# Performance work log

Measured on AMD Instinct MI355X. Metric: run time of the kernel, lower is better.

## Reference

```python
import jax, jax.numpy as jnp
import numpy as np

WS = 7        # window size
MAXD = 3      # correlation max displacement -> (2*3+1)^2 = 49 channels
T = 8         # hardcoded temporal length in forward
NUM_HEADS = 8


def setup_inputs() -> dict:
    key = jax.random.key(0)
    ks = jax.random.split(key, 5)
    B, H, W, C = 2, 56, 56, 128
    N = T * H * W
    x = jax.random.normal(ks[0], (B, N, C), jnp.float32)
    qkv_w = jax.random.normal(ks[1], (3 * C, C), jnp.float32) * 0.02
    proj_w = jax.random.normal(ks[2], (C, C), jnp.float32) * 0.02
    proj_b = jnp.zeros((C,), jnp.float32)
    pos_embed1 = jax.random.normal(ks[3], (1, WS * WS, 49), jnp.float32) * 0.02
    pos_embed2 = jax.random.normal(ks[4], (1, WS * WS, C // NUM_HEADS), jnp.float32) * 0.02
    return dict(x=x, qkv_w=qkv_w, proj_w=proj_w, proj_b=proj_b,
                pos_embed1=pos_embed1, pos_embed2=pos_embed2)


def _l2norm(x, axis):
    return x / jnp.maximum(jnp.sqrt(jnp.sum(x * x, axis=axis, keepdims=True)), 1e-12)


def _correlation(a, b):
    # a, b: (B, C, H, W) -> (B, H, W, 49); zero-padded shifted dot products over C
    Bc, Cc, H, W = a.shape
    bp = jnp.pad(b, ((0, 0), (0, 0), (MAXD, MAXD), (MAXD, MAXD)))
    outs = [jnp.sum(a * bp[:, :, du:du + H, dv:dv + W], axis=1)
            for du in range(2 * MAXD + 1) for dv in range(2 * MAXD + 1)]
    return jnp.stack(outs, axis=-1)


def _windows(x):
    # x: (B, H, W, D) -> (B*nh*nw, WS*WS, D); H split as (WS, nh) per torch reshape
    Bc, H, W, D = x.shape
    nh, nw = H // WS, W // WS
    x = x.reshape(Bc, WS, nh, WS, nw, D).transpose(0, 2, 4, 1, 3, 5)
    return x.reshape(Bc * nh * nw, WS * WS, D)


def _unwindows(x, Bc, H, W):
    nh, nw = H // WS, W // WS
    D = x.shape[-1]
    x = x.reshape(Bc, nh, nw, WS, WS, D).transpose(0, 3, 1, 4, 2, 5)
    return x.reshape(Bc, H, W, D)


def reference(x, qkv_w, proj_w, proj_b, pos_embed1, pos_embed2):
    B, N, C = x.shape
    H = int(np.sqrt(N // T)); W = H
    hd = C // NUM_HEADS
    BT = B * NUM_HEADS * T

    qkv = (x @ qkv_w.T).reshape(B, N, 3, NUM_HEADS, hd).transpose(2, 0, 3, 1, 4)
    q, k, v = qkv[0], qkv[1], qkv[2]            # (B, heads, N, hd)

    q = q.reshape(B * NUM_HEADS, T, H, W, hd).transpose(0, 1, 4, 2, 3)  # (B*h, T, hd, H, W)
    k = k.reshape(B * NUM_HEADS, T, H, W, hd).transpose(0, 1, 4, 2, 3)
    v = v.reshape(BT, H * W, hd)

    k_post = jnp.concatenate([k[:, 1:], k[:, -1:]], axis=1)  # shift by one frame
    qp = _l2norm(q.reshape(BT, hd, H, W), axis=1)
    kp = _l2norm(k_post.reshape(BT, hd, H, W), axis=1)

    corr = _correlation(qp, kp)                 # (BT, H, W, 49)
    corr = _windows(corr) + pos_embed1          # (BT*nh*nw, 49, 49)
    motion_attn = jax.nn.softmax(jnp.einsum('bnd,bmd->bnm', corr, corr), axis=-1)

    motion_v = _windows(v.reshape(BT, H, W, hd))
    motion_x = _unwindows(motion_attn @ motion_v, BT, H, W)

    qw = _windows(qp.transpose(0, 2, 3, 1)) + pos_embed2
    app_attn = jax.nn.softmax(jnp.einsum('bnd,bmd->bnm', qw, qw), axis=-1)
    app_x = _unwindows(app_attn @ motion_v, BT, H, W)

    out = 0.5 * app_x + 0.5 * motion_x          # (BT, H, W, hd)
    out = out.reshape(B, NUM_HEADS, T, H, W, hd).transpose(0, 2, 3, 4, 1, 5).reshape(B, N, C)
    return out @ proj_w.T + proj_b
```

## Files before the change

### kernel.cpp

```cpp
#include <hip/hip_runtime.h>
#include <math.h>

constexpr int H_   = 56;
constexpr int HW_  = 56 * 56;
constexpr int NPIX = 8 * HW_;
constexpr int SLAB = 128 * HW_ * 16;
constexpr int CWST = 52;

typedef __attribute__((ext_vector_type(8))) short bf16x8;
typedef __attribute__((ext_vector_type(4))) float f32x4;
typedef __attribute__((ext_vector_type(4))) unsigned int u32x4;

__device__ __forceinline__ unsigned short f2bf(float x) {
  unsigned int u = __float_as_uint(x);
  unsigned int r = (u + 0x7fffu + ((u >> 16) & 1u)) >> 16;
  return (unsigned short)r;
}
__device__ __forceinline__ float bf2f(unsigned short h) {
  return __uint_as_float(((unsigned int)h) << 16);
}

template <int MODE>
__global__ __launch_bounds__(256, 3) void gemm128(
    const float* X, const float* __restrict__ Wt, const float* __restrict__ bias,
    float* __restrict__ Yq, float* __restrict__ Yk, float* __restrict__ Yv,
    float* Yout)
{
  __shared__ float xT[32][132];
  __shared__ float wT[32][132];
  const int tid = threadIdx.x;
  const int tx = tid & 15, ty = tid >> 4;
  const int mbase = blockIdx.x * 128;
  const int nt = (MODE == 0) ? (int)blockIdx.y : 0;
  const float* Wp = Wt + (size_t)nt * (128 * 128);

  float acc[8][8];
#pragma unroll
  for (int i = 0; i < 8; ++i)
#pragma unroll
    for (int j = 0; j < 8; ++j) acc[i][j] = 0.f;

  const int srow = tid >> 3;
  const int scol = (tid & 7) * 4;

  for (int kt = 0; kt < 4; ++kt) {
    if (kt) __syncthreads();
#pragma unroll
    for (int p = 0; p < 4; ++p) {
      int r = p * 32 + srow;
      float4 vx = *(const float4*)&X [(size_t)(mbase + r) * 128 + kt * 32 + scol];
      float4 vw = *(const float4*)&Wp[(size_t)r * 128 + kt * 32 + scol];
      xT[scol + 0][r] = vx.x; xT[scol + 1][r] = vx.y; xT[scol + 2][r] = vx.z; xT[scol + 3][r] = vx.w;
      wT[scol + 0][r] = vw.x; wT[scol + 1][r] = vw.y; wT[scol + 2][r] = vw.z; wT[scol + 3][r] = vw.w;
    }
    __syncthreads();
#pragma unroll 4
    for (int c = 0; c < 32; ++c) {
      float4 a0 = *(const float4*)&xT[c][tx * 4];
      float4 a1 = *(const float4*)&xT[c][64 + tx * 4];
      float4 b0 = *(const float4*)&wT[c][ty * 4];
      float4 b1 = *(const float4*)&wT[c][64 + ty * 4];
      float a[8] = {a0.x, a0.y, a0.z, a0.w, a1.x, a1.y, a1.z, a1.w};
      float b[8] = {b0.x, b0.y, b0.z, b0.w, b1.x, b1.y, b1.z, b1.w};
#pragma unroll
      for (int i = 0; i < 8; ++i)
#pragma unroll
        for (int j = 0; j < 8; ++j) acc[i][j] += a[i] * b[j];
    }
  }

  if (MODE == 0) {
    const int hq = ty >> 2;
    const int cq = (ty & 3) * 4;
    float* Ybase = (nt == 0) ? Yq : ((nt == 1) ? Yk : Yv);
#pragma unroll
    for (int i = 0; i < 8; ++i) {
      int gpix = mbase + ((i < 4) ? (tx * 4 + i) : (64 + tx * 4 + (i - 4)));
      int b = gpix / NPIX;
      int rem = gpix - b * NPIX;
      int t = rem / HW_;
      int s = rem - t * HW_;
      float s0 = acc[i][0]*acc[i][0] + acc[i][1]*acc[i][1] + acc[i][2]*acc[i][2] + acc[i][3]*acc[i][3];
      float s1 = acc[i][4]*acc[i][4] + acc[i][5]*acc[i][5] + acc[i][6]*acc[i][6] + acc[i][7]*acc[i][7];
      s0 += __shfl_xor(s0, 16); s0 += __shfl_xor(s0, 32);
      s1 += __shfl_xor(s1, 16); s1 += __shfl_xor(s1, 32);
      float r0 = 1.f, r1 = 1.f;
      if (nt < 2) {
        r0 = 1.f / fmaxf(sqrtf(s0), 1e-12f);
        r1 = 1.f / fmaxf(sqrtf(s1), 1e-12f);
      }
      int bt0 = (b * 8 + hq) * 8 + t;
      int bt1 = (b * 8 + hq + 4) * 8 + t;
      float* d0 = Ybase + ((size_t)bt0 * HW_ + s) * 16 + cq;
      float* d1 = Ybase + ((size_t)bt1 * HW_ + s) * 16 + cq;
      *(float4*)d0 = make_float4(acc[i][0]*r0, acc[i][1]*r0, acc[i][2]*r0, acc[i][3]*r0);
      *(float4*)d1 = make_float4(acc[i][4]*r1, acc[i][5]*r1, acc[i][6]*r1, acc[i][7]*r1);
    }
  } else {
    float4 bb0 = *(const float4*)&bias[ty * 4];
    float4 bb1 = *(const float4*)&bias[64 + ty * 4];
#pragma unroll
    for (int i = 0; i < 8; ++i) {
      int gpix = mbase + ((i < 4) ? (tx * 4 + i) : (64 + tx * 4 + (i - 4)));
      float* dst = Yout + (size_t)gpix * 128;
      *(float4*)&dst[ty * 4]      = make_float4(acc[i][0]+bb0.x, acc[i][1]+bb0.y, acc[i][2]+bb0.z, acc[i][3]+bb0.w);
      *(float4*)&dst[64 + ty * 4] = make_float4(acc[i][4]+bb1.x, acc[i][5]+bb1.y, acc[i][6]+bb1.z, acc[i][7]+bb1.w);
    }
  }
}

__global__ __launch_bounds__(256) void corr_dense(
    const float* __restrict__ qn, const float* __restrict__ kn,
    const float* __restrict__ pos1,
    unsigned int* __restrict__ cwpk, float* __restrict__ diib)
{
  __shared__ float kS[10][56][16];
  const int bid = blockIdx.x;
  const int xcd = bid & 7;
  const int j = bid >> 3;
  const int g = j / 14;
  const int strip = j - g * 14;
  const int bt = xcd * 16 + g;
  const int h0 = strip * 4;
  const int t = bt & 7;
  const int btk = bt - t + ((t < 7) ? (t + 1) : 7);
  const float* qb = qn + (size_t)bt  * (HW_ * 16);
  const float* kb = kn + (size_t)btk * (HW_ * 16);
  const int tid = threadIdx.x;

  for (int idx = tid; idx < 2240; idx += 256) {
    int r = idx / 224;
    int c = idx - r * 224;
    int hh = h0 - 3 + r;
    f32x4 v = (f32x4)0.f;
    if ((unsigned)hh < 56u)
      v = *(const f32x4*)(kb + (size_t)(hh * 56) * 16 + c * 4);
    *(f32x4*)(&kS[r][0][0] + c * 4) = v;
  }
  __syncthreads();

  if (tid < 224) {
    const int py = tid / 56;
    const int h = h0 + py;
    const int w = tid - py * 56;
    const f32x4* qp = (const f32x4*)(qb + (size_t)(h * 56 + w) * 16);
    f32x4 q0 = qp[0], q1 = qp[1], q2 = qp[2], q3 = qp[3];
    const int ridx = (h >> 3) * 7 + (w >> 3);
    const float* p1r = pos1 + ridx * 49;
    unsigned int* outr = cwpk + (size_t)(bt * HW_ + h * 56 + w) * CWST;
    float dii = 0.f;
#pragma unroll
    for (int d4 = 0; d4 < 12; ++d4) {
      unsigned int pk[4];
#pragma unroll
      for (int e = 0; e < 4; ++e) {
        const int d = d4 * 4 + e;
        const int du = d / 7, dv = d % 7;
        const int ww = w + dv - 3;
        float val = 0.f;
        if (((unsigned)(h + du - 3) < 56u) && ((unsigned)ww < 56u)) {
          const f32x4* kp = (const f32x4*)&kS[py + du][ww][0];
          f32x4 a = q0 * kp[0] + q1 * kp[1] + q2 * kp[2] + q3 * kp[3];
          val = (a.x + a.y) + (a.z + a.w);
        }
        val += p1r[d];
        dii += val * val;
        unsigned short hb = f2bf(val);
        unsigned short lb = f2bf(val - bf2f(hb));
        pk[e] = (unsigned)hb | ((unsigned)lb << 16);
      }
      *(u32x4*)(outr + d4 * 4) = *(const u32x4*)pk;
    }
    {
      const int ww = w + 3;
      float val = 0.f;
      if (((unsigned)(h + 3) < 56u) && ((unsigned)ww < 56u)) {
        const f32x4* kp = (const f32x4*)&kS[py + 6][ww][0];
        f32x4 a = q0 * kp[0] + q1 * kp[1] + q2 * kp[2] + q3 * kp[3];
        val = (a.x + a.y) + (a.z + a.w);
      }
      val += p1r[48];
      dii += val * val;
      unsigned short hb = f2bf(val);
      unsigned short lb = f2bf(val - bf2f(hb));
      outr[48] = (unsigned)hb | ((unsigned)lb << 16);
    }
    diib[bt * HW_ + h * 56 + w] = dii;
  }
}

__global__ __launch_bounds__(64, 2) void attn_mfma(
    const float* __restrict__ qn, const float* __restrict__ vv,
    const unsigned int* __restrict__ cwpk, const float* __restrict__ diib,
    const float* __restrict__ pos2, float* __restrict__ mid)
{
  __shared__ __align__(16) unsigned char smem[7808];
  unsigned short* Pb   = (unsigned short*)smem;
  float*          mi_s = (float*)(smem + 7104);
  float*          scm  = (float*)(smem + 7300);
  float*          sca  = (float*)(smem + 7500);

  const int lane = threadIdx.x;
  const int lg = lane >> 4;
  const int lr = lane & 15;
  const int bid = blockIdx.x;
  const int xcd = bid & 7;
  const int j = bid >> 3;
  const int bt = xcd * 16 + (j >> 6);
  const int win = j & 63;
  const int wy = win >> 3;
  const int wx = win & 7;
  const float* qb = qn + (size_t)bt * (HW_ * 16);
  const float* vb = vv + (size_t)bt * (HW_ * 16);
  const unsigned int* cwb = cwpk + (size_t)bt * HW_ * CWST;
  const float* dib = diib + (size_t)bt * HW_;

  const bool rowok = (lane < 49);
  const int il = rowok ? lane : 48;

  float xv[2][8];
#pragma unroll
  for (int ks = 0; ks < 2; ++ks) {
#pragma unroll
    for (int e = 0; e < 8; ++e) {
      int k = ks * 32 + lg * 8 + e;
      int kc2 = (k < 49) ? k : 0;
      int ka = (kc2 * 37) >> 8;
      int kb2 = kc2 - ka * 7;
      float x = vb[(size_t)((ka * 8 + wy) * 56 + (kb2 * 8 + wx)) * 16 + lr];
      xv[ks][e] = (k < 49) ? x : 0.f;
    }
  }

  {
    const int ia = (il * 37) >> 8;
    const int ib = il - ia * 7;
    float dii = dib[(ia * 8 + wy) * 56 + (ib * 8 + wx)];
    float md = dii;
#pragma unroll
    for (int o = 32; o >= 1; o >>= 1) md = fmaxf(md, __shfl_xor(md, o));
    if (rowok) mi_s[il] = sqrtf(dii * md);
  }

  bf16x8 ah[4][2], al[4][2];
#pragma unroll
  for (int half = 0; half < 2; ++half) {
    u32x4 raw[2][2][2];
#pragma unroll
    for (int u = 0; u < 2; ++u) {
      const int tt2 = half * 2 + u;
      const int row = tt2 * 16 + lr;
      const int rowc = (row < 49) ? row : 0;
      const int a2 = (rowc * 37) >> 8;
      const int b3 = rowc - a2 * 7;
      const unsigned int* src = cwb + (size_t)((a2 * 8 + wy) * 56 + (b3 * 8 + wx)) * CWST;
#pragma unroll
      for (int ks = 0; ks < 2; ++ks) {
        const int cb = ks * 32 + lg * 8;
        raw[u][ks][0] = *(const u32x4*)(src + cb);
        raw[u][ks][1] = *(const u32x4*)(src + cb + 4);
      }
    }
#pragma unroll
    for (int u = 0; u < 2; ++u) {
      const int tt2 = half * 2 + u;
      const int row = tt2 * 16 + lr;
      const bool rv = (row < 49);
#pragma unroll
      for (int ks = 0; ks < 2; ++ks) {
        const int cb = ks * 32 + lg * 8;
        unsigned int u0[8];
        *(u32x4*)&u0[0] = raw[u][ks][0];
        *(u32x4*)&u0[4] = raw[u][ks][1];
#pragma unroll
        for (int e = 0; e < 8; ++e)
          if (!rv || (cb + e) >= 49) u0[e] = 0u;
        union { u32x4 uu; bf16x8 s; } Hh, Ll;
#pragma unroll
        for (int p = 0; p < 4; ++p) {
          Hh.uu[p] = (u0[2*p] & 0xffffu) | (u0[2*p+1] << 16);
          Ll.uu[p] = (u0[2*p] >> 16) | (u0[2*p+1] & 0xffff0000u);
        }
        ah[tt2][ks] = Hh.s;
        al[tt2][ks] = Ll.s;
      }
    }
  }

#pragma unroll
  for (int rt = 0; rt < 4; ++rt) {
    f32x4 C[4];
#pragma unroll
    for (int ct = 0; ct < 4; ++ct) C[ct] = (f32x4)0.f;
#pragma unroll
    for (int ks = 0; ks < 2; ++ks) {
#pragma unroll
      for (int ct = 0; ct < 4; ++ct) {
        C[ct] = __builtin_amdgcn_mfma_f32_16x16x32_bf16(ah[rt][ks], ah[ct][ks], C[ct], 0, 0, 0);
        C[ct] = __builtin_amdgcn_mfma_f32_16x16x32_bf16(ah[rt][ks], al[ct][ks], C[ct], 0, 0, 0);
        C[ct] = __builtin_amdgcn_mfma_f32_16x16x32_bf16(al[rt][ks], ah[ct][ks], C[ct], 0, 0, 0);
      }
    }
#pragma unroll
    for (int reg = 0; reg < 4; ++reg) {
      int row = rt * 16 + lg * 4 + reg;
      float m = mi_s[(row < 49) ? row : 0];
#pragma unroll
      for (int ct = 0; ct < 4; ++ct) {
        float p = __expf(C[ct][reg] - m);
        if (row < 49) Pb[row * 72 + ct * 16 + lr] = f2bf(p);
      }
    }
  }
  asm volatile("" ::: "memory");

  if (rowok) {
    const u32x4* pr = (const u32x4*)(Pb + il * 72);
    unsigned int uu[28];
#pragma unroll
    for (int w = 0; w < 7; ++w) *(u32x4*)&uu[4*w] = pr[w];
    float s = 0.f;
#pragma unroll
    for (int w = 0; w < 24; ++w)
      s += bf2f((unsigned short)(uu[w] & 0xffffu)) + bf2f((unsigned short)(uu[w] >> 16));
    s += bf2f((unsigned short)(uu[24] & 0xffffu));
    scm[il] = 0.5f / s;
  }

  bf16x8 vfh[2], vfl[2];
#pragma unroll
  for (int ks = 0; ks < 2; ++ks) {
    union { u32x4 u; bf16x8 s; } Hh, Ll;
#pragma unroll
    for (int p = 0; p < 4; ++p) {
      unsigned short h0 = f2bf(xv[ks][2*p]);
      unsigned short h1 = f2bf(xv[ks][2*p+1]);
      unsigned short l0 = f2bf(xv[ks][2*p]   - bf2f(h0));
      unsigned short l1 = f2bf(xv[ks][2*p+1] - bf2f(h1));
      Hh.u[p] = (unsigned int)h0 | ((unsigned int)h1 << 16);
      Ll.u[p] = (unsigned int)l0 | ((unsigned int)l1 << 16);
    }
    vfh[ks] = Hh.s;
    vfl[ks] = Ll.s;
  }

  f32x4 om[4];
#pragma unroll
  for (int rt = 0; rt < 4; ++rt) om[rt] = (f32x4)0.f;
#pragma unroll
  for (int ks = 0; ks < 2; ++ks) {
#pragma unroll
    for (int rt = 0; rt < 4; ++rt) {
      int row = rt * 16 + lr;
      int rowc = (row < 49) ? row : 0;
      bf16x8 pa = *(const bf16x8*)(Pb + rowc * 72 + ks * 32 + lg * 8);
      om[rt] = __builtin_amdgcn_mfma_f32_16x16x32_bf16(pa, vfh[ks], om[rt], 0, 0, 0);
      om[rt] = __builtin_amdgcn_mfma_f32_16x16x32_bf16(pa, vfl[ks], om[rt], 0, 0, 0);
    }
  }
  asm volatile("s_waitcnt lgkmcnt(0)" ::: "memory");

  bf16x8 qf[4];
#pragma unroll
  for (int half = 0; half < 2; ++half) {
    f32x4 qa_[2], qb_[2], pa_[2], pb_[2];
#pragma unroll
    for (int u = 0; u < 2; ++u) {
      const int tt2 = half * 2 + u;
      int row = tt2 * 16 + lr;
      int rowc = (row < 49) ? row : 0;
      int a2 = (rowc * 37) >> 8;
      int b3 = rowc - a2 * 7;
      const int co = (lg & 1) * 8;
      const float* qsrc = qb + (size_t)((a2 * 8 + wy) * 56 + (b3 * 8 + wx)) * 16 + co;
      qa_[u] = *(const f32x4*)qsrc;
      qb_[u] = *(const f32x4*)(qsrc + 4);
      const float* p2 = pos2 + rowc * 16 + co;
      pa_[u] = *(const f32x4*)p2;
      pb_[u] = *(const f32x4*)(p2 + 4);
    }
#pragma unroll
    for (int u = 0; u < 2; ++u) {
      const int tt2 = half * 2 + u;
      int row = tt2 * 16 + lr;
      f32x4 w0 = qa_[u] + pa_[u], w1 = qb_[u] + pb_[u];
      float ws[8] = {w0.x, w0.y, w0.z, w0.w, w1.x, w1.y, w1.z, w1.w};
      const bool zv = (row >= 49) || (lg >= 2);
      union { u32x4 u4; bf16x8 s; } Q;
#pragma unroll
      for (int p = 0; p < 4; ++p) {
        unsigned int v = (unsigned)f2bf(ws[2*p]) | ((unsigned)f2bf(ws[2*p+1]) << 16);
        Q.u4[p] = zv ? 0u : v;
      }
      qf[tt2] = Q.s;
    }
  }

#pragma unroll
  for (int rt = 0; rt < 4; ++rt) {
    f32x4 Ca[4];
#pragma unroll
    for (int ct = 0; ct < 4; ++ct) Ca[ct] = (f32x4)0.f;
#pragma unroll
    for (int ct = 0; ct < 4; ++ct)
      Ca[ct] = __builtin_amdgcn_mfma_f32_16x16x32_bf16(qf[rt], qf[ct], Ca[ct], 0, 0, 0);
#pragma unroll
    for (int reg = 0; reg < 4; ++reg) {
      int row = rt * 16 + lg * 4 + reg;
#pragma unroll
      for (int ct = 0; ct < 4; ++ct) {
        float p = __expf(Ca[ct][reg]);
        if (row < 49) Pb[row * 72 + ct * 16 + lr] = f2bf(p);
      }
    }
  }
  asm volatile("" ::: "memory");

  if (rowok) {
    const u32x4* pr = (const u32x4*)(Pb + il * 72);
    unsigned int uu[28];
#pragma unroll
    for (int w = 0; w < 7; ++w) *(u32x4*)&uu[4*w] = pr[w];
    float s = 0.f;
#pragma unroll
    for (int w = 0; w < 24; ++w)
      s += bf2f((unsigned short)(uu[w] & 0xffffu)) + bf2f((unsigned short)(uu[w] >> 16));
    s += bf2f((unsigned short)(uu[24] & 0xffffu));
    sca[il] = 0.5f / s;
  }

  f32x4 oa[4];
#pragma unroll
  for (int rt = 0; rt < 4; ++rt) oa[rt] = (f32x4)0.f;
#pragma unroll
  for (int ks = 0; ks < 2; ++ks) {
#pragma unroll
    for (int rt = 0; rt < 4; ++rt) {
      int row = rt * 16 + lr;
      int rowc = (row < 49) ? row : 0;
      bf16x8 pa = *(const bf16x8*)(Pb + rowc * 72 + ks * 32 + lg * 8);
      oa[rt] = __builtin_amdgcn_mfma_f32_16x16x32_bf16(pa, vfh[ks], oa[rt], 0, 0, 0);
      oa[rt] = __builtin_amdgcn_mfma_f32_16x16x32_bf16(pa, vfl[ks], oa[rt], 0, 0, 0);
    }
  }

  {
    int b = bt >> 6, e = (bt >> 3) & 7, tt = bt & 7;
    size_t obase = ((size_t)(b * NPIX + tt * HW_)) * 128 + e * 16 + lr;
#pragma unroll
    for (int rt = 0; rt < 4; ++rt) {
#pragma unroll
      for (int reg = 0; reg < 4; ++reg) {
        int row = rt * 16 + lg * 4 + reg;
        if (row < 49) {
          float o = om[rt][reg] * scm[row] + oa[rt][reg] * sca[row];
          int a2 = (row * 37) >> 8;
          int b3 = row - a2 * 7;
          mid[obase + (size_t)((a2 * 8 + wy) * 56 + (b3 * 8 + wx)) * 128] = o;
        }
      }
    }
  }
}

extern "C" void kernel_launch(void* const* d_in, const int* in_sizes, int n_in,
                              void* d_out, int out_size, void* d_ws, size_t ws_size,
                              hipStream_t stream) {
  (void)in_sizes; (void)n_in; (void)out_size; (void)ws_size;
  const float* x      = (const float*)d_in[0];
  const float* qkv_w  = (const float*)d_in[1];
  const float* proj_w = (const float*)d_in[2];
  const float* proj_b = (const float*)d_in[3];
  const float* pos1   = (const float*)d_in[4];
  const float* pos2   = (const float*)d_in[5];
  float* out = (float*)d_out;

  float* qn = (float*)d_ws;
  float* kc = qn + SLAB;
  float* vv = kc + SLAB;
  unsigned int* cwpk = (unsigned int*)(vv + SLAB);
  float* diib = (float*)(cwpk + (size_t)128 * HW_ * CWST + 64);

  gemm128<0><<<dim3(392, 3), 256, 0, stream>>>(x, qkv_w, nullptr, qn, kc, vv, nullptr);
  corr_dense<<<dim3(1792), 256, 0, stream>>>(qn, kc, pos1, cwpk, diib);
  attn_mfma<<<dim3(8192), 64, 0, stream>>>(qn, vv, cwpk, diib, pos2, out);
  gemm128<1><<<dim3(392), 256, 0, stream>>>(out, proj_w, proj_b, nullptr, nullptr, nullptr, out);
}
```

Baseline: 217.0 us.

## Store correlation output window-contiguous and stage it via LDS in attention

The correlation kernel now splits each pixel's 16-channel dot product across 4 lanes, reading K straight from global memory with clamped indices and combining partials with shuffles. It transposes results through LDS so the output is written in a per-window contiguous layout. The attention kernel then copies each window's 49x52 correlation tile into LDS with coalesced vector loads, replacing scattered per-row gathers. This trades the K-tile LDS reuse and one extra LDS pass for coalesced global traffic, and raises attention LDS use, which may lower occupancy.

```diff
diff --git a/kernel.cpp b/kernel.cpp
--- a/kernel.cpp
+++ b/kernel.cpp
@@ -5,7 +5,8 @@
 constexpr int HW_  = 56 * 56;
 constexpr int NPIX = 8 * HW_;
 constexpr int SLAB = 128 * HW_ * 16;
-constexpr int CWST = 52;
+constexpr int WINSZ = 49 * 52;
+constexpr int BTSZ  = 64 * WINSZ;
 
 typedef __attribute__((ext_vector_type(8))) short bf16x8;
 typedef __attribute__((ext_vector_type(4))) float f32x4;
@@ -18,6 +19,9 @@
 }
 __device__ __forceinline__ float bf2f(unsigned short h) {
   return __uint_as_float(((unsigned int)h) << 16);
+}
+__device__ __forceinline__ int clamp55(int v) {
+  return v < 0 ? 0 : (v > 55 ? 55 : v);
 }
 
 template <int MODE>
@@ -114,78 +118,101 @@
     const float* __restrict__ pos1,
     unsigned int* __restrict__ cwpk, float* __restrict__ diib)
 {
-  __shared__ float kS[10][56][16];
+  __shared__ unsigned int st[52 * 113 + 112];
+  const int tid = threadIdx.x;
+  const int c4 = tid & 3;
+  const int pl = tid >> 2;
   const int bid = blockIdx.x;
   const int xcd = bid & 7;
   const int j = bid >> 3;
-  const int g = j / 14;
-  const int strip = j - g * 14;
+  const int g = j / 28;
+  const int strip = j - g * 28;
   const int bt = xcd * 16 + g;
-  const int h0 = strip * 4;
+  const int h0 = strip * 2;
+  const int a2 = h0 >> 3;
+  const int wy0 = h0 & 7;
+  const int win0 = wy0 * 8;
   const int t = bt & 7;
   const int btk = bt - t + ((t < 7) ? (t + 1) : 7);
   const float* qb = qn + (size_t)bt  * (HW_ * 16);
   const float* kb = kn + (size_t)btk * (HW_ * 16);
-  const int tid = threadIdx.x;
-
-  for (int idx = tid; idx < 2240; idx += 256) {
-    int r = idx / 224;
-    int c = idx - r * 224;
-    int hh = h0 - 3 + r;
-    f32x4 v = (f32x4)0.f;
-    if ((unsigned)hh < 56u)
-      v = *(const f32x4*)(kb + (size_t)(hh * 56) * 16 + c * 4);
-    *(f32x4*)(&kS[r][0][0] + c * 4) = v;
-  }
-  __syncthreads();
-
-  if (tid < 224) {
-    const int py = tid / 56;
+
+#pragma unroll 1
+  for (int pass = 0; pass < 2; ++pass) {
+    const int p = pass * 64 + pl;
+    const bool act = (p < 112);
+    const int pc = act ? p : 0;
+    const int py = (pc >= 56) ? 1 : 0;
+    const int w = pc - py * 56;
     const int h = h0 + py;
-    const int w = tid - py * 56;
-    const f32x4* qp = (const f32x4*)(qb + (size_t)(h * 56 + w) * 16);
-    f32x4 q0 = qp[0], q1 = qp[1], q2 = qp[2], q3 = qp[3];
-    const int ridx = (h >> 3) * 7 + (w >> 3);
-    const float* p1r = pos1 + ridx * 49;
-    unsigned int* outr = cwpk + (size_t)(bt * HW_ + h * 56 + w) * CWST;
+    const int b3 = w >> 3, wx = w & 7;
+    const int slot = (py * 8 + wx) * 7 + b3;
+    const int row = a2 * 7 + b3;
+    const float* p1r = pos1 + row * 49;
+    const f32x4 qv = *(const f32x4*)(qb + (size_t)(h * 56 + w) * 16 + c4 * 4);
+    const bool wr = act && (c4 == 0);
     float dii = 0.f;
 #pragma unroll
-    for (int d4 = 0; d4 < 12; ++d4) {
-      unsigned int pk[4];
-#pragma unroll
-      for (int e = 0; e < 4; ++e) {
-        const int d = d4 * 4 + e;
+    for (int dbase = 0; dbase < 48; dbase += 8) {
+      f32x4 kv[8];
+#pragma unroll
+      for (int e = 0; e < 8; ++e) {
+        const int d = dbase + e;
         const int du = d / 7, dv = d % 7;
-        const int ww = w + dv - 3;
-        float val = 0.f;
-        if (((unsigned)(h + du - 3) < 56u) && ((unsigned)ww < 56u)) {
-          const f32x4* kp = (const f32x4*)&kS[py + du][ww][0];
-          f32x4 a = q0 * kp[0] + q1 * kp[1] + q2 * kp[2] + q3 * kp[3];
-          val = (a.x + a.y) + (a.z + a.w);
+        const int hc = clamp55(h + du - 3);
+        const int wc = clamp55(w + dv - 3);
+        kv[e] = *(const f32x4*)(kb + (size_t)(hc * 56 + wc) * 16 + c4 * 4);
+      }
+#pragma unroll
+      for (int e = 0; e < 8; ++e) {
+        const int d = dbase + e;
+        const int du = d / 7, dv = d % 7;
+        const int hh = h + du - 3, ww = w + dv - 3;
+        float pd = fmaf(qv.x, kv[e].x, fmaf(qv.y, kv[e].y, fmaf(qv.z, kv[e].z, qv.w * kv[e].w)));
+        pd = ((unsigned)hh < 56u && (unsigned)ww < 56u) ? pd : 0.f;
+        pd += __shfl_xor(pd, 1);
+        pd += __shfl_xor(pd, 2);
+        const float val = pd + p1r[d];
+        dii += val * val;
+        if (wr) {
+          unsigned short hb = f2bf(val);
+          unsigned short lb = f2bf(val - bf2f(hb));
+          st[d * 113 + slot] = (unsigned)hb | ((unsigned)lb << 16);
         }
-        val += p1r[d];
-        dii += val * val;
+      }
+    }
+    {
+      const int hh = h + 3, ww = w + 3;
+      float pd = 0.f;
+      if ((unsigned)hh < 56u && (unsigned)ww < 56u) {
+        const f32x4 kv = *(const f32x4*)(kb + (size_t)(hh * 56 + ww) * 16 + c4 * 4);
+        pd = fmaf(qv.x, kv.x, fmaf(qv.y, kv.y, fmaf(qv.z, kv.z, qv.w * kv.w)));
+      }
+      pd += __shfl_xor(pd, 1);
+      pd += __shfl_xor(pd, 2);
+      const float val = pd + p1r[48];
+      dii += val * val;
+      if (wr) {
         unsigned short hb = f2bf(val);
         unsigned short lb = f2bf(val - bf2f(hb));
-        pk[e] = (unsigned)hb | ((unsigned)lb << 16);
-      }
-      *(u32x4*)(outr + d4 * 4) = *(const u32x4*)pk;
-    }
-    {
-      const int ww = w + 3;
-      float val = 0.f;
-      if (((unsigned)(h + 3) < 56u) && ((unsigned)ww < 56u)) {
-        const f32x4* kp = (const f32x4*)&kS[py + 6][ww][0];
-        f32x4 a = q0 * kp[0] + q1 * kp[1] + q2 * kp[2] + q3 * kp[3];
-        val = (a.x + a.y) + (a.z + a.w);
-      }
-      val += p1r[48];
-      dii += val * val;
-      unsigned short hb = f2bf(val);
-      unsigned short lb = f2bf(val - bf2f(hb));
-      outr[48] = (unsigned)hb | ((unsigned)lb << 16);
-    }
-    diib[bt * HW_ + h * 56 + w] = dii;
+        st[48 * 113 + slot] = (unsigned)hb | ((unsigned)lb << 16);
+        st[49 * 113 + slot] = 0u;
+        st[50 * 113 + slot] = 0u;
+        st[51 * 113 + slot] = 0u;
+        diib[bt * HW_ + h * 56 + w] = dii;
+      }
+    }
+  }
+  __syncthreads();
+
+  unsigned int* gw = cwpk + (size_t)bt * BTSZ + (size_t)win0 * WINSZ + a2 * 364;
+#pragma unroll 1
+  for (int f = tid; f < 5824; f += 256) {
+    const int wl = f / 364;
+    const int r = f - wl * 364;
+    const int d = r % 52;
+    const int b3 = r / 52;
+    gw[wl * WINSZ + r] = st[d * 113 + wl * 7 + b3];
   }
 }
 
@@ -194,11 +221,12 @@
     const unsigned int* __restrict__ cwpk, const float* __restrict__ diib,
     const float* __restrict__ pos2, float* __restrict__ mid)
 {
-  __shared__ __align__(16) unsigned char smem[7808];
+  __shared__ __align__(16) unsigned char smem[10840];
+  unsigned int*   cwS  = (unsigned int*)smem;
   unsigned short* Pb   = (unsigned short*)smem;
-  float*          mi_s = (float*)(smem + 7104);
-  float*          scm  = (float*)(smem + 7300);
-  float*          sca  = (float*)(smem + 7500);
+  float*          mi_s = (float*)(smem + 10240);
+  float*          scm  = (float*)(smem + 10440);
+  float*          sca  = (float*)(smem + 10640);
 
   const int lane = threadIdx.x;
   const int lg = lane >> 4;
@@ -212,11 +240,20 @@
   const int wx = win & 7;
   const float* qb = qn + (size_t)bt * (HW_ * 16);
   const float* vb = vv + (size_t)bt * (HW_ * 16);
-  const unsigned int* cwb = cwpk + (size_t)bt * HW_ * CWST;
   const float* dib = diib + (size_t)bt * HW_;
 
   const bool rowok = (lane < 49);
   const int il = rowok ? lane : 48;
+
+  {
+    const u32x4* src = (const u32x4*)(cwpk + (size_t)bt * BTSZ + (size_t)win * WINSZ);
+    u32x4* dst = (u32x4*)cwS;
+#pragma unroll
+    for (int it = 0; it < 10; ++it) {
+      int f = it * 64 + lane;
+      if (f < 637) dst[f] = src[f];
+    }
+  }
 
   float xv[2][8];
 #pragma unroll
@@ -241,51 +278,35 @@
     for (int o = 32; o >= 1; o >>= 1) md = fmaxf(md, __shfl_xor(md, o));
     if (rowok) mi_s[il] = sqrtf(dii * md);
   }
+  asm volatile("s_waitcnt lgkmcnt(0)" ::: "memory");
 
   bf16x8 ah[4][2], al[4][2];
 #pragma unroll
-  for (int half = 0; half < 2; ++half) {
-    u32x4 raw[2][2][2];
-#pragma unroll
-    for (int u = 0; u < 2; ++u) {
-      const int tt2 = half * 2 + u;
+  for (int tt2 = 0; tt2 < 4; ++tt2) {
+#pragma unroll
+    for (int ks = 0; ks < 2; ++ks) {
       const int row = tt2 * 16 + lr;
       const int rowc = (row < 49) ? row : 0;
-      const int a2 = (rowc * 37) >> 8;
-      const int b3 = rowc - a2 * 7;
-      const unsigned int* src = cwb + (size_t)((a2 * 8 + wy) * 56 + (b3 * 8 + wx)) * CWST;
-#pragma unroll
-      for (int ks = 0; ks < 2; ++ks) {
-        const int cb = ks * 32 + lg * 8;
-        raw[u][ks][0] = *(const u32x4*)(src + cb);
-        raw[u][ks][1] = *(const u32x4*)(src + cb + 4);
-      }
-    }
-#pragma unroll
-    for (int u = 0; u < 2; ++u) {
-      const int tt2 = half * 2 + u;
-      const int row = tt2 * 16 + lr;
+      const int cb = ks * 32 + lg * 8;
+      const unsigned int* s2 = cwS + rowc * 52 + cb;
+      unsigned int u0[8];
+      *(u32x4*)&u0[0] = *(const u32x4*)s2;
+      *(u32x4*)&u0[4] = *(const u32x4*)(s2 + 4);
       const bool rv = (row < 49);
 #pragma unroll
-      for (int ks = 0; ks < 2; ++ks) {
-        const int cb = ks * 32 + lg * 8;
-        unsigned int u0[8];
-        *(u32x4*)&u0[0] = raw[u][ks][0];
-        *(u32x4*)&u0[4] = raw[u][ks][1];
-#pragma unroll
-        for (int e = 0; e < 8; ++e)
-          if (!rv || (cb + e) >= 49) u0[e] = 0u;
-        union { u32x4 uu; bf16x8 s; } Hh, Ll;
-#pragma unroll
-        for (int p = 0; p < 4; ++p) {
-          Hh.uu[p] = (u0[2*p] & 0xffffu) | (u0[2*p+1] << 16);
-          Ll.uu[p] = (u0[2*p] >> 16) | (u0[2*p+1] & 0xffff0000u);
-        }
-        ah[tt2][ks] = Hh.s;
-        al[tt2][ks] = Ll.s;
-      }
-    }
-  }
+      for (int e = 0; e < 8; ++e)
+        if (!rv || (cb + e) >= 49) u0[e] = 0u;
+      union { u32x4 uu; bf16x8 s; } Hh, Ll;
+#pragma unroll
+      for (int p = 0; p < 4; ++p) {
+        Hh.uu[p] = (u0[2*p] & 0xffffu) | (u0[2*p+1] << 16);
+        Ll.uu[p] = (u0[2*p] >> 16) | (u0[2*p+1] & 0xffff0000u);
+      }
+      ah[tt2][ks] = Hh.s;
+      al[tt2][ks] = Ll.s;
+    }
+  }
+  asm volatile("s_waitcnt lgkmcnt(0)" ::: "memory");
 
 #pragma unroll
   for (int rt = 0; rt < 4; ++rt) {
@@ -479,10 +500,10 @@
   float* kc = qn + SLAB;
   float* vv = kc + SLAB;
   unsigned int* cwpk = (unsigned int*)(vv + SLAB);
-  float* diib = (float*)(cwpk + (size_t)128 * HW_ * CWST + 64);
+  float* diib = (float*)(cwpk + (size_t)128 * BTSZ + 64);
 
   gemm128<0><<<dim3(392, 3), 256, 0, stream>>>(x, qkv_w, nullptr, qn, kc, vv, nullptr);
-  corr_dense<<<dim3(1792), 256, 0, stream>>>(qn, kc, pos1, cwpk, diib);
+  corr_dense<<<dim3(3584), 256, 0, stream>>>(qn, kc, pos1, cwpk, diib);
   attn_mfma<<<dim3(8192), 64, 0, stream>>>(qn, vv, cwpk, diib, pos2, out);
   gemm128<1><<<dim3(392), 256, 0, stream>>>(out, proj_w, proj_b, nullptr, nullptr, nullptr, out);
 }
```

New measurement: 240.3 us. 10.8% more time.
